# Kernel optimization log

Hardware: AMD Instinct MI355X
Metric: run time of the kernel (lower is better)

The kernel has to match this reference:

```python
import jax, jax.numpy as jnp
import numpy as np

N = 50000       # num nodes
E = 400000      # num edges (before self loops)
IN, HID, H, OUT = 128, 64, 4, 64
SLOPE = 0.2     # PyG GATv2Conv default negative_slope


def setup_inputs() -> dict:
    key = jax.random.key(0)
    ks = jax.random.split(key, 14)
    def lin(k, fan_in, fan_out):
        return jax.random.normal(k, (fan_in, fan_out), jnp.float32) / np.sqrt(fan_in)
    return {
        "x": jax.random.normal(ks[0], (N, IN), jnp.float32),
        "edge_index": jax.random.randint(ks[1], (2, E), 0, N, jnp.int32),
        # layer 1: in=IN -> HID per head, H heads, concat
        "Wl1": lin(ks[2], IN, H * HID), "bl1": jnp.zeros((H * HID,), jnp.float32),
        "Wr1": lin(ks[3], IN, H * HID), "br1": jnp.zeros((H * HID,), jnp.float32),
        "att1": jax.random.normal(ks[4], (H, HID), jnp.float32) / np.sqrt(HID),
        "bias1": jnp.zeros((H * HID,), jnp.float32),
        # layer 2: in=H*HID -> OUT, 1 head, concat=False
        "Wl2": lin(ks[5], H * HID, OUT), "bl2": jnp.zeros((OUT,), jnp.float32),
        "Wr2": lin(ks[6], H * HID, OUT), "br2": jnp.zeros((OUT,), jnp.float32),
        "att2": jax.random.normal(ks[7], (1, OUT), jnp.float32) / np.sqrt(OUT),
        "bias2": jnp.zeros((OUT,), jnp.float32),
    }


def gatv2_conv(x, src, dst, Wl, bl, Wr, br, att, heads, out_ch, num_nodes):
    """PyG GATv2Conv (share_weights=False). src->dst aggregation at dst."""
    xl = (x @ Wl + bl).reshape(-1, heads, out_ch)  # source transform (x_j)
    xr = (x @ Wr + br).reshape(-1, heads, out_ch)  # target transform (x_i)
    m = xl[src] + xr[dst]                          # [E, H, C]
    e = jnp.sum(jax.nn.leaky_relu(m, SLOPE) * att, axis=-1)  # [E, H]
    # segment softmax over incoming edges of each dst node
    emax = jax.ops.segment_max(e, dst, num_segments=num_nodes)
    ex = jnp.exp(e - emax[dst])
    denom = jax.ops.segment_sum(ex, dst, num_segments=num_nodes)
    alpha = ex / denom[dst]                        # [E, H]
    out = jax.ops.segment_sum(alpha[:, :, None] * xl[src], dst, num_segments=num_nodes)
    return out  # [N, H, C]


def reference(x, edge_index, Wl1, bl1, Wr1, br1, att1, bias1,
              Wl2, bl2, Wr2, br2, att2, bias2):
    n = x.shape[0]
    loops = jnp.arange(n, dtype=edge_index.dtype)
    src = jnp.concatenate([edge_index[0], loops])  # add_self_loops=True
    dst = jnp.concatenate([edge_index[1], loops])
    h = gatv2_conv(x, src, dst, Wl1, bl1, Wr1, br1, att1, H, HID, n)
    h = h.reshape(n, H * HID) + bias1              # concat=True
    h = jax.nn.elu(h)                              # dropout=0.0
    o = gatv2_conv(h, src, dst, Wl2, bl2, Wr2, br2, att2, 1, OUT, n)
    return o.reshape(n, OUT) + bias2               # concat=False, heads=1
```

## Files before the change

kernel.cpp:

```cpp
#include <hip/hip_runtime.h>
#include <hip/hip_bf16.h>

typedef unsigned short u16;
typedef __attribute__((ext_vector_type(8))) short short8;
typedef __attribute__((ext_vector_type(4))) float floatx4;
typedef __attribute__((ext_vector_type(2))) float f32x2;

#define N_NODES 50000
#define N_EDGES 400000
#define ET      450000
#define F_IN    128
#define C1      256
#define HID     64
#define OUTC    64
#define SLOPE   0.2f
#define LIN1_BLOCKS 782
#define LIN1_GEMM   1564
#define LOG2E   1.44269504089f

#if __has_builtin(__builtin_amdgcn_exp2f)
#define EXP2(x) __builtin_amdgcn_exp2f(x)
#else
#define EXP2(x) __expf((x) * 0.69314718056f)
#endif

__device__ __forceinline__ float bf2f(u16 v) {
    return __uint_as_float(((unsigned)v) << 16);
}
__device__ __forceinline__ float bflo(unsigned u) { return __uint_as_float(u << 16); }
__device__ __forceinline__ float bfhi(unsigned u) { return __uint_as_float(u & 0xffff0000u); }
__device__ __forceinline__ u16 f2bf(float f) {
    unsigned u = __float_as_uint(f);
    return (u16)((u + 0x7fffu + ((u >> 16) & 1u)) >> 16);
}
__device__ __forceinline__ f32x2 up2(unsigned u) {
    f32x2 r; r.x = bflo(u); r.y = bfhi(u); return r;
}
template<int CTRL>
__device__ __forceinline__ float dpp_add(float x) {
    return x + __int_as_float(__builtin_amdgcn_update_dpp(
        0, __float_as_int(x), CTRL, 0xF, 0xF, true));
}
__device__ __forceinline__ float red16(float p) {
    p = dpp_add<0xB1>(p);
    p = dpp_add<0x4E>(p);
    p = dpp_add<0x141>(p);
    p = dpp_add<0x140>(p);
    return p;
}
template<int CTRL>
__device__ __forceinline__ f32x2 dpp_add2(f32x2 x) {
    f32x2 o;
    o.x = __int_as_float(__builtin_amdgcn_update_dpp(
        0, __float_as_int(x.x), CTRL, 0xF, 0xF, true));
    o.y = __int_as_float(__builtin_amdgcn_update_dpp(
        0, __float_as_int(x.y), CTRL, 0xF, 0xF, true));
    return x + o;
}
__device__ __forceinline__ f32x2 red16x2(f32x2 p) {
    p = dpp_add2<0xB1>(p);
    p = dpp_add2<0x4E>(p);
    p = dpp_add2<0x141>(p);
    p = dpp_add2<0x140>(p);
    return p;
}
__device__ __forceinline__ bool detect_f32(const unsigned* __restrict__ xw) {
    unsigned w = xw[threadIdx.x & 63];
    unsigned aexp = (w >> 7) & 0xFFu;
    unsigned long long b = __ballot(aexp >= 170u || aexp <= 40u);
    return __popcll(b) >= 16;
}

__global__ __launch_bounds__(256) void convert_all_kernel(
    const unsigned* __restrict__ xw,
    const void* wl1, const void* wr1, const void* wl2, const void* wr2,
    const void* s0, const void* s1, const void* s2, const void* s3,
    const void* s4, const void* s5, const void* s6, const void* s7,
    u16* __restrict__ wt, u16* __restrict__ prm, int* __restrict__ hist)
{
    if (blockIdx.x >= 385) {
        int idx = (blockIdx.x - 385) * 256 + threadIdx.x;
        if (idx < N_NODES) hist[idx] = 0;
        return;
    }
    bool f32m = detect_f32(xw);
    if (blockIdx.x == 384) {
        for (int t = threadIdx.x; t < 1280; t += 256) {
            const void* src; int local;
            if      (t < 256)  { src = s0; local = t; }
            else if (t < 512)  { src = s1; local = t - 256; }
            else if (t < 768)  { src = s2; local = t - 512; }
            else if (t < 1024) { src = s3; local = t - 768; }
            else if (t < 1088) { src = s4; local = t - 1024; }
            else if (t < 1152) { src = s5; local = t - 1088; }
            else if (t < 1216) { src = s6; local = t - 1152; }
            else               { src = s7; local = t - 1216; }
            prm[t] = f32m ? f2bf(((const float*)src)[local]) : ((const u16*)src)[local];
        }
        return;
    }
    int t = blockIdx.x * 256 + threadIdx.x;
    const void* src; int local, k, n, K, base;
    if (t < 32768)      { src = wl1; local = t;         k = local >> 8; n = local & 255; K = 128; base = 0; }
    else if (t < 65536) { src = wr1; local = t - 32768; k = local >> 8; n = local & 255; K = 128; base = 32768; }
    else if (t < 81920) { src = wl2; local = t - 65536; k = local >> 6; n = local & 63;  K = 256; base = 65536; }
    else                { src = wr2; local = t - 81920; k = local >> 6; n = local & 63;  K = 256; base = 81920; }
    u16 v = f32m ? f2bf(((const float*)src)[local]) : ((const u16*)src)[local];
    wt[base + n * K + k] = v;
}

__global__ __launch_bounds__(256) void scan1_kernel(const int* __restrict__ hist,
                                                    int* __restrict__ rowptr,
                                                    int* __restrict__ bsum)
{
    int t = threadIdx.x;
    int i = blockIdx.x * 256 + t;
    int v = (i < N_NODES) ? hist[i] : 0;
    __shared__ int sd[256];
    sd[t] = v;
    __syncthreads();
    #pragma unroll
    for (int ofs = 1; ofs < 256; ofs <<= 1) {
        int u = (t >= ofs) ? sd[t - ofs] : 0;
        __syncthreads();
        sd[t] += u;
        __syncthreads();
    }
    if (i < N_NODES) rowptr[i] = sd[t] - v;
    if (t == 255) bsum[blockIdx.x] = sd[255];
}

__global__ __launch_bounds__(256) void scan3_kernel(int* __restrict__ rowptr,
                                                    const int* __restrict__ bsum,
                                                    int* __restrict__ off)
{
    int t = threadIdx.x;
    int v = (t < (int)blockIdx.x) ? bsum[t] : 0;
    __shared__ int sd[256];
    sd[t] = v;
    __syncthreads();
    #pragma unroll
    for (int ofs = 1; ofs < 256; ofs <<= 1) {
        int u = (t >= ofs) ? sd[t - ofs] : 0;
        __syncthreads();
        sd[t] += u;
        __syncthreads();
    }
    int boff = sd[255];
    int i = blockIdx.x * 256 + t;
    if (i < N_NODES) {
        int r = rowptr[i] + boff;
        rowptr[i] = r;
        off[i] = r;
    }
}

__global__ __launch_bounds__(256) void scatter_kernel(const int* __restrict__ ei,
                                                      int* __restrict__ off,
                                                      int* __restrict__ src_csr)
{
    int t = blockIdx.x * 256 + threadIdx.x;
    if (t >= ET) return;
    int s, d;
    if (t < N_EDGES) { s = ei[t]; d = ei[N_EDGES + t]; } else { s = d = t - N_EDGES; }
    int pos = atomicAdd(&off[d], 1);
    src_csr[pos] = s;
}

__global__ __launch_bounds__(256) void lin1_hist_kernel(
    const u16* __restrict__ X, const u16* __restrict__ Wt,
    const u16* __restrict__ bl, const u16* __restrict__ br,
    u16* __restrict__ Yl, u16* __restrict__ Yr, int nrows,
    const int* __restrict__ ei, int* __restrict__ hist)
{
    constexpr int K = 128, N = 256, LS = K + 8;
    __shared__ __align__(16) u16 sX[64 * LS];
    __shared__ __align__(16) u16 sW[64 * LS];

    if (blockIdx.x >= LIN1_GEMM) {
        int t = (blockIdx.x - LIN1_GEMM) * 256 + threadIdx.x;
        if (t < ET) {
            int d = (t < N_EDGES) ? ei[N_EDGES + t] : t - N_EDGES;
            atomicAdd(&hist[d], 1);
        }
        return;
    }

    const bool f32m = detect_f32((const unsigned*)X);
    const float* X32 = (const float*)X;
    const int side = blockIdx.x & 1;
    const int row0 = (blockIdx.x >> 1) * 64;
    const int wave = threadIdx.x >> 6, lane = threadIdx.x & 63;
    const int quad = lane >> 4, l16 = lane & 15;

    for (int i = threadIdx.x * 8; i < 64 * K; i += 2048) {
        int r = i >> 7, c = i & 127;
        int gr = row0 + r;
        u16* dst = &sX[r * LS + c];
        if (f32m) {
            float4 v0 = make_float4(0.f, 0.f, 0.f, 0.f), v1 = v0;
            if (gr < nrows) {
                v0 = *(const float4*)&X32[(size_t)gr * K + c];
                v1 = *(const float4*)&X32[(size_t)gr * K + c + 4];
            }
            ushort4 p0, p1;
            p0.x = f2bf(v0.x); p0.y = f2bf(v0.y); p0.z = f2bf(v0.z); p0.w = f2bf(v0.w);
            p1.x = f2bf(v1.x); p1.y = f2bf(v1.y); p1.z = f2bf(v1.z); p1.w = f2bf(v1.w);
            *(ushort4*)dst = p0;
            *(ushort4*)(dst + 4) = p1;
        } else {
            uint4 v = {0u, 0u, 0u, 0u};
            if (gr < nrows) v = *(const uint4*)&X[(size_t)gr * K + c];
            *(uint4*)dst = v;
        }
    }
    __syncthreads();

    short8 a[4];
    #pragma unroll
    for (int kk = 0; kk < 4; ++kk)
        a[kk] = *(const short8*)&sX[(wave * 16 + l16) * LS + kk * 32 + quad * 8];

    const u16* wbase = Wt + side * (N * K);
    const u16* bias  = side ? br : bl;
    u16* Y = side ? Yr : Yl;
    for (int ch = 0; ch < 4; ++ch) {
        if (ch) __syncthreads();
        for (int i = threadIdx.x * 8; i < 64 * K; i += 2048) {
            int n = i >> 7, c = i & 127;
            *(uint4*)&sW[n * LS + c] = *(const uint4*)&wbase[(size_t)(ch * 64 + n) * K + c];
        }
        __syncthreads();
        floatx4 acc0 = {0.f, 0.f, 0.f, 0.f}, acc1 = acc0, acc2 = acc0, acc3 = acc0;
        #pragma unroll
        for (int kk = 0; kk < 4; ++kk) {
            short8 b0 = *(const short8*)&sW[(l16) * LS + kk * 32 + quad * 8];
            short8 b1 = *(const short8*)&sW[(16 + l16) * LS + kk * 32 + quad * 8];
            short8 b2 = *(const short8*)&sW[(32 + l16) * LS + kk * 32 + quad * 8];
            short8 b3 = *(const short8*)&sW[(48 + l16) * LS + kk * 32 + quad * 8];
            acc0 = __builtin_amdgcn_mfma_f32_16x16x32_bf16(a[kk], b0, acc0, 0, 0, 0);
            acc1 = __builtin_amdgcn_mfma_f32_16x16x32_bf16(a[kk], b1, acc1, 0, 0, 0);
            acc2 = __builtin_amdgcn_mfma_f32_16x16x32_bf16(a[kk], b2, acc2, 0, 0, 0);
            acc3 = __builtin_amdgcn_mfma_f32_16x16x32_bf16(a[kk], b3, acc3, 0, 0, 0);
        }
        const int rbase = row0 + wave * 16 + quad * 4;
        #pragma unroll
        for (int cf = 0; cf < 4; ++cf) {
            const floatx4 av = (cf == 0) ? acc0 : (cf == 1) ? acc1 : (cf == 2) ? acc2 : acc3;
            const int col = ch * 64 + cf * 16 + l16;
            const float bv = bf2f(bias[col]);
            #pragma unroll
            for (int r = 0; r < 4; ++r) {
                int row = rbase + r;
                if (row < nrows) Y[(size_t)row * N + col] = f2bf(av[r] + bv);
            }
        }
    }
}

__global__ __launch_bounds__(256) void lin2_fused_kernel(
    const u16* __restrict__ X, const u16* __restrict__ Wt,
    const u16* __restrict__ bl, const u16* __restrict__ br,
    u16* __restrict__ Yl, u16* __restrict__ Yr, int nrows)
{
    constexpr int K = 256, N = 64, LS = K + 8;
    __shared__ __align__(16) u16 sX[64 * LS];
    __shared__ __align__(16) u16 sW[64 * LS];
    const int row0 = blockIdx.x * 64;
    const int wave = threadIdx.x >> 6, lane = threadIdx.x & 63;
    const int quad = lane >> 4, l16 = lane & 15;

    for (int i = threadIdx.x * 8; i < 64 * K; i += 2048) {
        int r = i >> 8, c = i & 255;
        int gr = row0 + r;
        uint4 v = {0u, 0u, 0u, 0u};
        if (gr < nrows) v = *(const uint4*)&X[(size_t)gr * K + c];
        *(uint4*)&sX[r * LS + c] = v;
    }
    __syncthreads();

    short8 a[8];
    #pragma unroll
    for (int kk = 0; kk < 8; ++kk)
        a[kk] = *(const short8*)&sX[(wave * 16 + l16) * LS + kk * 32 + quad * 8];

    for (int side = 0; side < 2; ++side) {
        const u16* wbase = Wt + side * (N * K);
        const u16* bias  = side ? br : bl;
        u16* Y = side ? Yr : Yl;
        __syncthreads();
        for (int i = threadIdx.x * 8; i < 64 * K; i += 2048) {
            int n = i >> 8, c = i & 255;
            *(uint4*)&sW[n * LS + c] = *(const uint4*)&wbase[(size_t)n * K + c];
        }
        __syncthreads();
        floatx4 acc0 = {0.f, 0.f, 0.f, 0.f}, acc1 = acc0, acc2 = acc0, acc3 = acc0;
        #pragma unroll
        for (int kk = 0; kk < 8; ++kk) {
            short8 b0 = *(const short8*)&sW[(l16) * LS + kk * 32 + quad * 8];
            short8 b1 = *(const short8*)&sW[(16 + l16) * LS + kk * 32 + quad * 8];
            short8 b2 = *(const short8*)&sW[(32 + l16) * LS + kk * 32 + quad * 8];
            short8 b3 = *(const short8*)&sW[(48 + l16) * LS + kk * 32 + quad * 8];
            acc0 = __builtin_amdgcn_mfma_f32_16x16x32_bf16(a[kk], b0, acc0, 0, 0, 0);
            acc1 = __builtin_amdgcn_mfma_f32_16x16x32_bf16(a[kk], b1, acc1, 0, 0, 0);
            acc2 = __builtin_amdgcn_mfma_f32_16x16x32_bf16(a[kk], b2, acc2, 0, 0, 0);
            acc3 = __builtin_amdgcn_mfma_f32_16x16x32_bf16(a[kk], b3, acc3, 0, 0, 0);
        }
        const int rbase = row0 + wave * 16 + quad * 4;
        #pragma unroll
        for (int cf = 0; cf < 4; ++cf) {
            const floatx4 av = (cf == 0) ? acc0 : (cf == 1) ? acc1 : (cf == 2) ? acc2 : acc3;
            const int col = cf * 16 + l16;
            const float bv = bf2f(bias[col]);
            #pragma unroll
            for (int r = 0; r < 4; ++r) {
                int row = rbase + r;
                if (row < nrows) Y[(size_t)row * N + col] = f2bf(av[r] + bv);
            }
        }
    }
}

__global__ __launch_bounds__(64, 6) void node1_kernel(
    const u16* __restrict__ xl, const u16* __restrict__ xr,
    const int* __restrict__ rowptr, const int* __restrict__ hist,
    const int* __restrict__ src_csr, const u16* __restrict__ att,
    const u16* __restrict__ bias, u16* __restrict__ hout)
{
    const int d = blockIdx.x;
    const int l = threadIdx.x;
    const int start = __builtin_amdgcn_readfirstlane(rowptr[d]);
    const int deg = __builtin_amdgcn_readfirstlane(hist[d]);
    const int dm1 = deg - 1;
    const u16* __restrict__ xlp = xl + l * 4;

    uint2 auv = *(const uint2*)&att[l * 4];
    const f32x2 atA = up2(auv.x) * LOG2E, atB = up2(auv.y) * LOG2E;
    uint2 ruv = *(const uint2*)&xr[(size_t)d * C1 + l * 4];
    const f32x2 rA = up2(ruv.x), rB = up2(ruv.y);

    float m = -1e30f, la = 0.f;
    f32x2 accA = {0.f, 0.f}, accB = {0.f, 0.f};

    int s0 = __builtin_amdgcn_readfirstlane(src_csr[start]);
    int s1 = __builtin_amdgcn_readfirstlane(src_csr[start + min(1, dm1)]);
    int s2 = __builtin_amdgcn_readfirstlane(src_csr[start + min(2, dm1)]);
    int s3 = __builtin_amdgcn_readfirstlane(src_csr[start + min(3, dm1)]);
    uint2 u0 = *(const uint2*)&xlp[(size_t)s0 * C1];
    uint2 u1 = *(const uint2*)&xlp[(size_t)s1 * C1];
    uint2 u2 = *(const uint2*)&xlp[(size_t)s2 * C1];
    uint2 u3 = *(const uint2*)&xlp[(size_t)s3 * C1];

    int j = 0;
    for (; j + 4 <= deg; j += 4) {
        const uint2 c0 = u0, c1 = u1, c2 = u2, c3 = u3;
        const int jn = j + 4;
        if (jn < deg) {
            int t0 = __builtin_amdgcn_readfirstlane(src_csr[start + jn]);
            int t1 = __builtin_amdgcn_readfirstlane(src_csr[start + min(jn + 1, dm1)]);
            int t2 = __builtin_amdgcn_readfirstlane(src_csr[start + min(jn + 2, dm1)]);
            int t3 = __builtin_amdgcn_readfirstlane(src_csr[start + min(jn + 3, dm1)]);
            u0 = *(const uint2*)&xlp[(size_t)t0 * C1];
            u1 = *(const uint2*)&xlp[(size_t)t1 * C1];
            u2 = *(const uint2*)&xlp[(size_t)t2 * C1];
            u3 = *(const uint2*)&xlp[(size_t)t3 * C1];
        }
        f32x2 x0A = up2(c0.x), x0B = up2(c0.y);
        f32x2 x1A = up2(c1.x), x1B = up2(c1.y);
        f32x2 x2A = up2(c2.x), x2B = up2(c2.y);
        f32x2 x3A = up2(c3.x), x3B = up2(c3.y);
        f32x2 t, pv;
        t = x0A + rA; t = __builtin_elementwise_max(t, t * SLOPE); pv  = t * atA;
        t = x0B + rB; t = __builtin_elementwise_max(t, t * SLOPE); pv += t * atB;
        float p0 = pv.x + pv.y;
        t = x1A + rA; t = __builtin_elementwise_max(t, t * SLOPE); pv  = t * atA;
        t = x1B + rB; t = __builtin_elementwise_max(t, t * SLOPE); pv += t * atB;
        float p1 = pv.x + pv.y;
        t = x2A + rA; t = __builtin_elementwise_max(t, t * SLOPE); pv  = t * atA;
        t = x2B + rB; t = __builtin_elementwise_max(t, t * SLOPE); pv += t * atB;
        float p2 = pv.x + pv.y;
        t = x3A + rA; t = __builtin_elementwise_max(t, t * SLOPE); pv  = t * atA;
        t = x3B + rB; t = __builtin_elementwise_max(t, t * SLOPE); pv += t * atB;
        float p3 = pv.x + pv.y;
        f32x2 P01 = {p0, p1}, P23 = {p2, p3};
        P01 = red16x2(P01);
        P23 = red16x2(P23);
        p0 = P01.x; p1 = P01.y; p2 = P23.x; p3 = P23.y;
        float pm = fmaxf(fmaxf(p0, p1), fmaxf(p2, p3));
        if (__any(pm > m)) {
            float mn = fmaxf(m, pm);
            float sc = EXP2(m - mn);
            la *= sc; accA *= sc; accB *= sc;
            m = mn;
        }
        float w0 = EXP2(p0 - m);
        float w1 = EXP2(p1 - m);
        float w2 = EXP2(p2 - m);
        float w3 = EXP2(p3 - m);
        la += w0 + w1 + w2 + w3;
        accA += x0A * w0 + x1A * w1 + x2A * w2 + x3A * w3;
        accB += x0B * w0 + x1B * w1 + x2B * w2 + x3B * w3;
    }
    if (j < deg) {
        const bool v1 = j + 1 < deg, v2 = j + 2 < deg;
        f32x2 x0A = up2(u0.x), x0B = up2(u0.y);
        f32x2 x1A = up2(u1.x), x1B = up2(u1.y);
        f32x2 x2A = up2(u2.x), x2B = up2(u2.y);
        f32x2 t, pv;
        t = x0A + rA; t = __builtin_elementwise_max(t, t * SLOPE); pv  = t * atA;
        t = x0B + rB; t = __builtin_elementwise_max(t, t * SLOPE); pv += t * atB;
        float p0 = pv.x + pv.y;
        t = x1A + rA; t = __builtin_elementwise_max(t, t * SLOPE); pv  = t * atA;
        t = x1B + rB; t = __builtin_elementwise_max(t, t * SLOPE); pv += t * atB;
        float p1 = pv.x + pv.y;
        t = x2A + rA; t = __builtin_elementwise_max(t, t * SLOPE); pv  = t * atA;
        t = x2B + rB; t = __builtin_elementwise_max(t, t * SLOPE); pv += t * atB;
        float p2 = pv.x + pv.y;
        f32x2 P01 = {p0, p1};
        P01 = red16x2(P01);
        p0 = P01.x; p1 = P01.y;
        p2 = red16(p2);
        float pm = p0;
        if (v1) pm = fmaxf(pm, p1);
        if (v2) pm = fmaxf(pm, p2);
        if (__any(pm > m)) {
            float mn = fmaxf(m, pm);
            float sc = EXP2(m - mn);
            la *= sc; accA *= sc; accB *= sc;
            m = mn;
        }
        float w0 = EXP2(p0 - m);
        float w1 = v1 ? EXP2(p1 - m) : 0.f;
        float w2 = v2 ? EXP2(p2 - m) : 0.f;
        la += w0 + w1 + w2;
        accA += x0A * w0 + x1A * w1 + x2A * w2;
        accB += x0B * w0 + x1B * w1 + x2B * w2;
    }
    const float inv = 1.f / la;
    const int c = l * 4;
    float v0 = accA.x * inv + bf2f(bias[c + 0]);
    float v1 = accA.y * inv + bf2f(bias[c + 1]);
    float v2 = accB.x * inv + bf2f(bias[c + 2]);
    float v3 = accB.y * inv + bf2f(bias[c + 3]);
    v0 = v0 > 0.f ? v0 : __expf(fminf(v0, 0.f)) - 1.f;
    v1 = v1 > 0.f ? v1 : __expf(fminf(v1, 0.f)) - 1.f;
    v2 = v2 > 0.f ? v2 : __expf(fminf(v2, 0.f)) - 1.f;
    v3 = v3 > 0.f ? v3 : __expf(fminf(v3, 0.f)) - 1.f;
    ushort4 o;
    o.x = f2bf(v0); o.y = f2bf(v1); o.z = f2bf(v2); o.w = f2bf(v3);
    *(ushort4*)&hout[(size_t)d * C1 + c] = o;
}

__global__ __launch_bounds__(64, 8) void node2_kernel(
    const u16* __restrict__ xl, const u16* __restrict__ xr,
    const int* __restrict__ rowptr, const int* __restrict__ hist,
    const int* __restrict__ src_csr, const u16* __restrict__ att,
    const u16* __restrict__ bias, void* __restrict__ outp,
    const unsigned* __restrict__ xorig)
{
    const bool f32o = detect_f32(xorig);
    const int d = blockIdx.x;
    const int l = threadIdx.x;
    const int start = __builtin_amdgcn_readfirstlane(rowptr[d]);
    const int deg = __builtin_amdgcn_readfirstlane(hist[d]);
    const int dm1 = deg - 1;
    const int g = l >> 4, sub = l & 15;
    const int c0 = sub * 4;
    const u16* __restrict__ xlp = xl + c0;

    uint2 auv = *(const uint2*)&att[c0];
    const f32x2 atA = up2(auv.x) * LOG2E, atB = up2(auv.y) * LOG2E;
    uint2 ruv = *(const uint2*)&xr[(size_t)d * OUTC + c0];
    const f32x2 rA = up2(ruv.x), rB = up2(ruv.y);

    float m = -1e30f, la = 0.f;
    f32x2 accA = {0.f, 0.f}, accB = {0.f, 0.f};

    int sA = src_csr[start + min(g, dm1)];
    uint2 uA = *(const uint2*)&xlp[(size_t)sA * OUTC];
    int sB = src_csr[start + min(4 + g, dm1)];
    uint2 uB = *(const uint2*)&xlp[(size_t)sB * OUTC];

    for (int j = 0; j < deg; j += 4) {
        const bool valid = j + g < deg;
        const uint2 uv = uA;
        uA = uB;
        {
            int sC = src_csr[start + min(j + 8 + g, dm1)];
            uB = *(const uint2*)&xlp[(size_t)sC * OUTC];
        }
        f32x2 xA = up2(uv.x), xB = up2(uv.y);
        f32x2 t, pv;
        t = xA + rA; t = __builtin_elementwise_max(t, t * SLOPE); pv  = t * atA;
        t = xB + rB; t = __builtin_elementwise_max(t, t * SLOPE); pv += t * atB;
        float p = pv.x + pv.y;
        p = red16(p);
        float pvv = valid ? p : -1e30f;
        if (__any(pvv > m)) {
            float mn = fmaxf(m, pvv);
            float sc = EXP2(m - mn);
            la *= sc; accA *= sc; accB *= sc;
            m = mn;
        }
        float w = valid ? EXP2(p - m) : 0.f;
        la += w;
        accA += xA * w;
        accB += xB * w;
    }
    #pragma unroll
    for (int ofs = 16; ofs <= 32; ofs <<= 1) {
        float mo = __shfl_xor(m, ofs);
        float lo = __shfl_xor(la, ofs);
        float bax = __shfl_xor(accA.x, ofs);
        float bay = __shfl_xor(accA.y, ofs);
        float bbx = __shfl_xor(accB.x, ofs);
        float bby = __shfl_xor(accB.y, ofs);
        float mn = fmaxf(m, mo);
        float e0 = EXP2(m - mn), e1 = EXP2(mo - mn);
        la = la * e0 + lo * e1;
        accA.x = accA.x * e0 + bax * e1;
        accA.y = accA.y * e0 + bay * e1;
        accB.x = accB.x * e0 + bbx * e1;
        accB.y = accB.y * e0 + bby * e1;
        m = mn;
    }
    if (g == 0) {
        const float inv = 1.f / la;
        float v0 = accA.x * inv + bf2f(bias[c0 + 0]);
        float v1 = accA.y * inv + bf2f(bias[c0 + 1]);
        float v2 = accB.x * inv + bf2f(bias[c0 + 2]);
        float v3 = accB.y * inv + bf2f(bias[c0 + 3]);
        if (f32o) {
            float4 o = make_float4(v0, v1, v2, v3);
            *(float4*)&((float*)outp)[(size_t)d * OUTC + c0] = o;
        } else {
            ushort4 o;
            o.x = f2bf(v0); o.y = f2bf(v1); o.z = f2bf(v2); o.w = f2bf(v3);
            *(ushort4*)&((u16*)outp)[(size_t)d * OUTC + c0] = o;
        }
    }
}

extern "C" void kernel_launch(void* const* d_in, const int* in_sizes, int n_in,
                              void* d_out, int out_size, void* d_ws, size_t ws_size,
                              hipStream_t stream)
{
    const void* x  = d_in[0];
    const int*  ei = (const int*)d_in[1];

    char* ws = (char*)d_ws;
    u16* xl1     = (u16*)(ws + 0);
    u16* xr1     = (u16*)(ws + 25600000);
    u16* hbuf    = (u16*)(ws + 51200000);
    u16* xl2     = (u16*)(ws + 0);
    u16* xr2     = (u16*)(ws + 6400000);
    int* hist    = (int*)(ws + 76800000);
    int* rowptr  = (int*)(ws + 77000000);
    int* off     = (int*)(ws + 77200000);
    int* src_csr = (int*)(ws + 77400000);
    u16* prm     = (u16*)(ws + 79200064);
    u16* wt      = (u16*)(ws + 79210240);
    int* bsum    = (int*)(ws + 79410000);

    u16* bl1   = prm + 0;
    u16* br1   = prm + 256;
    u16* att1  = prm + 512;
    u16* bias1 = prm + 768;
    u16* bl2   = prm + 1024;
    u16* br2   = prm + 1088;
    u16* att2  = prm + 1152;
    u16* bias2 = prm + 1216;
    u16* wt1   = wt + 0;
    u16* wt2   = wt + 65536;

    convert_all_kernel<<<581, 256, 0, stream>>>(
        (const unsigned*)x,
        d_in[2], d_in[4], d_in[8], d_in[10],
        d_in[3], d_in[5], d_in[6], d_in[7], d_in[9], d_in[11], d_in[12], d_in[13],
        wt, prm, hist);

    const int eb = (ET + 255) / 256;
    lin1_hist_kernel<<<LIN1_GEMM + eb, 256, 0, stream>>>(
        (const u16*)x, wt1, bl1, br1, xl1, xr1, N_NODES, ei, hist);

    scan1_kernel<<<196, 256, 0, stream>>>(hist, rowptr, bsum);
    scan3_kernel<<<196, 256, 0, stream>>>(rowptr, bsum, off);
    scatter_kernel<<<eb, 256, 0, stream>>>(ei, off, src_csr);

    node1_kernel<<<N_NODES, 64, 0, stream>>>(xl1, xr1, rowptr, hist, src_csr, att1, bias1, hbuf);
    lin2_fused_kernel<<<(N_NODES + 63) / 64, 256, 0, stream>>>(hbuf, wt2, bl2, br2, xl2, xr2, N_NODES);
    node2_kernel<<<N_NODES, 64, 0, stream>>>(xl2, xr2, rowptr, hist, src_csr, att2, bias2, d_out,
                                             (const unsigned*)x);
}
```

Before: 249.7 us.

## Drop LDS staging in linear GEMMs; per-wave tiles load operands directly from global

Both linear-layer kernels now give each wave an independent 16-row by side tile. The wave reads its X fragments and weight fragments straight from global memory into registers, with no shared-memory staging and no block barriers. The MFMA operands are swapped so each lane writes four contiguous output columns as one vector store, replacing scattered 2-byte stores. In exchange, weights are re-read from global or L2 by every wave with no LDS reuse, and the bounds checks on row count are removed because 50000 divides evenly into 16-row tiles.

```diff
diff --git a/kernel.cpp b/kernel.cpp
--- a/kernel.cpp
+++ b/kernel.cpp
@@ -14,8 +14,9 @@
 #define HID     64
 #define OUTC    64
 #define SLOPE   0.2f
-#define LIN1_BLOCKS 782
-#define LIN1_GEMM   1564
+#define LIN1_WAVES 6250
+#define LIN1_GEMMB 1563
+#define LIN2_GEMMB 1563
 #define LOG2E   1.44269504089f
 
 #if __has_builtin(__builtin_amdgcn_exp2f)
@@ -170,15 +171,11 @@
 __global__ __launch_bounds__(256) void lin1_hist_kernel(
     const u16* __restrict__ X, const u16* __restrict__ Wt,
     const u16* __restrict__ bl, const u16* __restrict__ br,
-    u16* __restrict__ Yl, u16* __restrict__ Yr, int nrows,
+    u16* __restrict__ Yl, u16* __restrict__ Yr,
     const int* __restrict__ ei, int* __restrict__ hist)
 {
-    constexpr int K = 128, N = 256, LS = K + 8;
-    __shared__ __align__(16) u16 sX[64 * LS];
-    __shared__ __align__(16) u16 sW[64 * LS];
-
-    if (blockIdx.x >= LIN1_GEMM) {
-        int t = (blockIdx.x - LIN1_GEMM) * 256 + threadIdx.x;
+    if (blockIdx.x >= LIN1_GEMMB) {
+        int t = (blockIdx.x - LIN1_GEMMB) * 256 + threadIdx.x;
         if (t < ET) {
             int d = (t < N_EDGES) ? ei[N_EDGES + t] : t - N_EDGES;
             atomicAdd(&hist[d], 1);
@@ -186,74 +183,69 @@
         return;
     }
 
-    const bool f32m = detect_f32((const unsigned*)X);
-    const float* X32 = (const float*)X;
-    const int side = blockIdx.x & 1;
-    const int row0 = (blockIdx.x >> 1) * 64;
     const int wave = threadIdx.x >> 6, lane = threadIdx.x & 63;
     const int quad = lane >> 4, l16 = lane & 15;
-
-    for (int i = threadIdx.x * 8; i < 64 * K; i += 2048) {
-        int r = i >> 7, c = i & 127;
-        int gr = row0 + r;
-        u16* dst = &sX[r * LS + c];
-        if (f32m) {
-            float4 v0 = make_float4(0.f, 0.f, 0.f, 0.f), v1 = v0;
-            if (gr < nrows) {
-                v0 = *(const float4*)&X32[(size_t)gr * K + c];
-                v1 = *(const float4*)&X32[(size_t)gr * K + c + 4];
-            }
-            ushort4 p0, p1;
-            p0.x = f2bf(v0.x); p0.y = f2bf(v0.y); p0.z = f2bf(v0.z); p0.w = f2bf(v0.w);
-            p1.x = f2bf(v1.x); p1.y = f2bf(v1.y); p1.z = f2bf(v1.z); p1.w = f2bf(v1.w);
-            *(ushort4*)dst = p0;
-            *(ushort4*)(dst + 4) = p1;
-        } else {
-            uint4 v = {0u, 0u, 0u, 0u};
-            if (gr < nrows) v = *(const uint4*)&X[(size_t)gr * K + c];
-            *(uint4*)dst = v;
-        }
-    }
-    __syncthreads();
+    const int w = blockIdx.x * 4 + wave;
+    if (w >= LIN1_WAVES) return;
+    const int side = w & 1;
+    const int row  = (w >> 1) * 16 + l16;
+
+    const bool f32m = detect_f32((const unsigned*)X);
 
     short8 a[4];
-    #pragma unroll
-    for (int kk = 0; kk < 4; ++kk)
-        a[kk] = *(const short8*)&sX[(wave * 16 + l16) * LS + kk * 32 + quad * 8];
-
-    const u16* wbase = Wt + side * (N * K);
+    if (f32m) {
+        const float* xrow = (const float*)X + (size_t)row * F_IN;
+        #pragma unroll
+        for (int kk = 0; kk < 4; ++kk) {
+            float4 v0 = *(const float4*)&xrow[kk * 32 + quad * 8];
+            float4 v1 = *(const float4*)&xrow[kk * 32 + quad * 8 + 4];
+            union { ushort4 h[2]; short8 s8; } u;
+            u.h[0].x = f2bf(v0.x); u.h[0].y = f2bf(v0.y);
+            u.h[0].z = f2bf(v0.z); u.h[0].w = f2bf(v0.w);
+            u.h[1].x = f2bf(v1.x); u.h[1].y = f2bf(v1.y);
+            u.h[1].z = f2bf(v1.z); u.h[1].w = f2bf(v1.w);
+            a[kk] = u.s8;
+        }
+    } else {
+        const u16* xrow = X + (size_t)row * F_IN;
+        #pragma unroll
+        for (int kk = 0; kk < 4; ++kk)
+            a[kk] = *(const short8*)&xrow[kk * 32 + quad * 8];
+    }
+
+    const u16* wside = Wt + side * (C1 * F_IN);
     const u16* bias  = side ? br : bl;
     u16* Y = side ? Yr : Yl;
+    u16* yrow = Y + (size_t)row * C1;
+
     for (int ch = 0; ch < 4; ++ch) {
-        if (ch) __syncthreads();
-        for (int i = threadIdx.x * 8; i < 64 * K; i += 2048) {
-            int n = i >> 7, c = i & 127;
-            *(uint4*)&sW[n * LS + c] = *(const uint4*)&wbase[(size_t)(ch * 64 + n) * K + c];
-        }
-        __syncthreads();
-        floatx4 acc0 = {0.f, 0.f, 0.f, 0.f}, acc1 = acc0, acc2 = acc0, acc3 = acc0;
-        #pragma unroll
-        for (int kk = 0; kk < 4; ++kk) {
-            short8 b0 = *(const short8*)&sW[(l16) * LS + kk * 32 + quad * 8];
-            short8 b1 = *(const short8*)&sW[(16 + l16) * LS + kk * 32 + quad * 8];
-            short8 b2 = *(const short8*)&sW[(32 + l16) * LS + kk * 32 + quad * 8];
-            short8 b3 = *(const short8*)&sW[(48 + l16) * LS + kk * 32 + quad * 8];
-            acc0 = __builtin_amdgcn_mfma_f32_16x16x32_bf16(a[kk], b0, acc0, 0, 0, 0);
-            acc1 = __builtin_amdgcn_mfma_f32_16x16x32_bf16(a[kk], b1, acc1, 0, 0, 0);
-            acc2 = __builtin_amdgcn_mfma_f32_16x16x32_bf16(a[kk], b2, acc2, 0, 0, 0);
-            acc3 = __builtin_amdgcn_mfma_f32_16x16x32_bf16(a[kk], b3, acc3, 0, 0, 0);
-        }
-        const int rbase = row0 + wave * 16 + quad * 4;
+        short8 b[16];
+        #pragma unroll
+        for (int cf = 0; cf < 4; ++cf)
+            #pragma unroll
+            for (int kk = 0; kk < 4; ++kk)
+                b[cf * 4 + kk] = *(const short8*)&wside[
+                    (size_t)(ch * 64 + cf * 16 + l16) * F_IN + kk * 32 + quad * 8];
+        floatx4 acc[4];
+        #pragma unroll
+        for (int cf = 0; cf < 4; ++cf) acc[cf] = (floatx4){0.f, 0.f, 0.f, 0.f};
+        #pragma unroll
+        for (int cf = 0; cf < 4; ++cf)
+            #pragma unroll
+            for (int kk = 0; kk < 4; ++kk)
+                acc[cf] = __builtin_amdgcn_mfma_f32_16x16x32_bf16(
+                    b[cf * 4 + kk], a[kk], acc[cf], 0, 0, 0);
         #pragma unroll
         for (int cf = 0; cf < 4; ++cf) {
-            const floatx4 av = (cf == 0) ? acc0 : (cf == 1) ? acc1 : (cf == 2) ? acc2 : acc3;
-            const int col = ch * 64 + cf * 16 + l16;
-            const float bv = bf2f(bias[col]);
-            #pragma unroll
-            for (int r = 0; r < 4; ++r) {
-                int row = rbase + r;
-                if (row < nrows) Y[(size_t)row * N + col] = f2bf(av[r] + bv);
-            }
+            const int col = ch * 64 + cf * 16 + quad * 4;
+            uint2 bu = *(const uint2*)&bias[col];
+            f32x2 b01 = up2(bu.x), b23 = up2(bu.y);
+            ushort4 o;
+            o.x = f2bf(acc[cf][0] + b01.x);
+            o.y = f2bf(acc[cf][1] + b01.y);
+            o.z = f2bf(acc[cf][2] + b23.x);
+            o.w = f2bf(acc[cf][3] + b23.y);
+            *(ushort4*)&yrow[col] = o;
         }
     }
 }
@@ -261,63 +253,46 @@
 __global__ __launch_bounds__(256) void lin2_fused_kernel(
     const u16* __restrict__ X, const u16* __restrict__ Wt,
     const u16* __restrict__ bl, const u16* __restrict__ br,
-    u16* __restrict__ Yl, u16* __restrict__ Yr, int nrows)
-{
-    constexpr int K = 256, N = 64, LS = K + 8;
-    __shared__ __align__(16) u16 sX[64 * LS];
-    __shared__ __align__(16) u16 sW[64 * LS];
-    const int row0 = blockIdx.x * 64;
+    u16* __restrict__ Yl, u16* __restrict__ Yr)
+{
     const int wave = threadIdx.x >> 6, lane = threadIdx.x & 63;
     const int quad = lane >> 4, l16 = lane & 15;
-
-    for (int i = threadIdx.x * 8; i < 64 * K; i += 2048) {
-        int r = i >> 8, c = i & 255;
-        int gr = row0 + r;
-        uint4 v = {0u, 0u, 0u, 0u};
-        if (gr < nrows) v = *(const uint4*)&X[(size_t)gr * K + c];
-        *(uint4*)&sX[r * LS + c] = v;
-    }
-    __syncthreads();
-
+    const int w = blockIdx.x * 4 + wave;
+    if (w >= LIN1_WAVES) return;
+    const int side = w & 1;
+    const int row  = (w >> 1) * 16 + l16;
+
+    const u16* xrow = X + (size_t)row * C1;
     short8 a[8];
     #pragma unroll
     for (int kk = 0; kk < 8; ++kk)
-        a[kk] = *(const short8*)&sX[(wave * 16 + l16) * LS + kk * 32 + quad * 8];
-
-    for (int side = 0; side < 2; ++side) {
-        const u16* wbase = Wt + side * (N * K);
-        const u16* bias  = side ? br : bl;
-        u16* Y = side ? Yr : Yl;
-        __syncthreads();
-        for (int i = threadIdx.x * 8; i < 64 * K; i += 2048) {
-            int n = i >> 8, c = i & 255;
-            *(uint4*)&sW[n * LS + c] = *(const uint4*)&wbase[(size_t)n * K + c];
-        }
-        __syncthreads();
-        floatx4 acc0 = {0.f, 0.f, 0.f, 0.f}, acc1 = acc0, acc2 = acc0, acc3 = acc0;
-        #pragma unroll
-        for (int kk = 0; kk < 8; ++kk) {
-            short8 b0 = *(const short8*)&sW[(l16) * LS + kk * 32 + quad * 8];
-            short8 b1 = *(const short8*)&sW[(16 + l16) * LS + kk * 32 + quad * 8];
-            short8 b2 = *(const short8*)&sW[(32 + l16) * LS + kk * 32 + quad * 8];
-            short8 b3 = *(const short8*)&sW[(48 + l16) * LS + kk * 32 + quad * 8];
-            acc0 = __builtin_amdgcn_mfma_f32_16x16x32_bf16(a[kk], b0, acc0, 0, 0, 0);
-            acc1 = __builtin_amdgcn_mfma_f32_16x16x32_bf16(a[kk], b1, acc1, 0, 0, 0);
-            acc2 = __builtin_amdgcn_mfma_f32_16x16x32_bf16(a[kk], b2, acc2, 0, 0, 0);
-            acc3 = __builtin_amdgcn_mfma_f32_16x16x32_bf16(a[kk], b3, acc3, 0, 0, 0);
-        }
-        const int rbase = row0 + wave * 16 + quad * 4;
-        #pragma unroll
-        for (int cf = 0; cf < 4; ++cf) {
-            const floatx4 av = (cf == 0) ? acc0 : (cf == 1) ? acc1 : (cf == 2) ? acc2 : acc3;
-            const int col = cf * 16 + l16;
-            const float bv = bf2f(bias[col]);
-            #pragma unroll
-            for (int r = 0; r < 4; ++r) {
-                int row = rbase + r;
-                if (row < nrows) Y[(size_t)row * N + col] = f2bf(av[r] + bv);
-            }
-        }
+        a[kk] = *(const short8*)&xrow[kk * 32 + quad * 8];
+
+    const u16* wside = Wt + side * (OUTC * C1);
+    const u16* bias  = side ? br : bl;
+    u16* Y = side ? Yr : Yl;
+    u16* yrow = Y + (size_t)row * OUTC;
+
+    #pragma unroll
+    for (int cf = 0; cf < 4; ++cf) {
+        short8 b[8];
+        #pragma unroll
+        for (int kk = 0; kk < 8; ++kk)
+            b[kk] = *(const short8*)&wside[
+                (size_t)(cf * 16 + l16) * C1 + kk * 32 + quad * 8];
+        floatx4 acc = {0.f, 0.f, 0.f, 0.f};
+        #pragma unroll
+        for (int kk = 0; kk < 8; ++kk)
+            acc = __builtin_amdgcn_mfma_f32_16x16x32_bf16(b[kk], a[kk], acc, 0, 0, 0);
+        const int col = cf * 16 + quad * 4;
+        uint2 bu = *(const uint2*)&bias[col];
+        f32x2 b01 = up2(bu.x), b23 = up2(bu.y);
+        ushort4 o;
+        o.x = f2bf(acc[0] + b01.x);
+        o.y = f2bf(acc[1] + b01.y);
+        o.z = f2bf(acc[2] + b23.x);
+        o.w = f2bf(acc[3] + b23.y);
+        *(ushort4*)&yrow[col] = o;
     }
 }
 
@@ -580,15 +555,15 @@
         wt, prm, hist);
 
     const int eb = (ET + 255) / 256;
-    lin1_hist_kernel<<<LIN1_GEMM + eb, 256, 0, stream>>>(
-        (const u16*)x, wt1, bl1, br1, xl1, xr1, N_NODES, ei, hist);
+    lin1_hist_kernel<<<LIN1_GEMMB + eb, 256, 0, stream>>>(
+        (const u16*)x, wt1, bl1, br1, xl1, xr1, ei, hist);
 
     scan1_kernel<<<196, 256, 0, stream>>>(hist, rowptr, bsum);
     scan3_kernel<<<196, 256, 0, stream>>>(rowptr, bsum, off);
     scatter_kernel<<<eb, 256, 0, stream>>>(ei, off, src_csr);
 
     node1_kernel<<<N_NODES, 64, 0, stream>>>(xl1, xr1, rowptr, hist, src_csr, att1, bias1, hbuf);
-    lin2_fused_kernel<<<(N_NODES + 63) / 64, 256, 0, stream>>>(hbuf, wt2, bl2, br2, xl2, xr2, N_NODES);
+    lin2_fused_kernel<<<LIN2_GEMMB, 256, 0, stream>>>(hbuf, wt2, bl2, br2, xl2, xr2);
     node2_kernel<<<N_NODES, 64, 0, stream>>>(xl2, xr2, rowptr, hist, src_csr, att2, bias2, d_out,
                                              (const unsigned*)x);
 }
```

Measured after the change: 291.6 us. +16.8%, slower.
